# Kernel optimization log

Measured on AMD Instinct MI355X. Metric: run time of the kernel, lower is better.

The kernel has to match this reference:

```python
import math
import jax, jax.numpy as jnp
import numpy as np

B, L, D = 2, 2048, 1024
NH = 16
HS = D // NH
BLOCK_SIZE = 2048


def setup_inputs() -> dict:
    key = jax.random.key(0)
    ks = jax.random.split(key, 4)
    x = jax.random.normal(ks[0], (B, L, D), dtype=jnp.float32)
    Wqkv = jax.random.normal(ks[1], (D, 3 * D), dtype=jnp.float32) * 0.02
    bqkv = jnp.zeros((3 * D,), dtype=jnp.float32)
    Wproj = jax.random.normal(ks[2], (D, D), dtype=jnp.float32) * 0.02
    bproj = jnp.zeros((D,), dtype=jnp.float32)
    Er = jax.random.normal(ks[3], (BLOCK_SIZE, HS), dtype=jnp.float32)
    return {"x": x, "Wqkv": Wqkv, "bqkv": bqkv, "Wproj": Wproj, "bproj": bproj, "Er": Er}


def _skew(QEr):
    # QEr: [B, nh, L, L]  (Music Transformer skew trick)
    b, nh, nr, nc = QEr.shape
    padded = jnp.pad(QEr, ((0, 0), (0, 0), (0, 0), (1, 0)))  # [B, nh, nr, nc+1]
    reshaped = padded.reshape(b, nh, nc + 1, nr)
    return reshaped[:, :, 1:, :]  # [B, nh, nr, nc]


def reference(x, Wqkv, bqkv, Wproj, bproj, Er):
    b, l, d = x.shape
    qkv = x @ Wqkv + bqkv  # [B, L, 3D]
    q, k, v = jnp.split(qkv, 3, axis=2)
    q = q.reshape(b, l, NH, HS).transpose(0, 2, 1, 3)  # [B, nh, L, hs]
    k = k.reshape(b, l, NH, HS).transpose(0, 2, 1, 3)
    v = v.reshape(b, l, NH, HS).transpose(0, 2, 1, 3)

    start = BLOCK_SIZE - l
    Er_t = Er[start:, :].T  # [hs, L]
    QEr = jnp.einsum('bhld,dm->bhlm', q, Er_t)  # [B, nh, L, L]
    Srel = _skew(QEr)

    QK_t = jnp.einsum('bhld,bhmd->bhlm', q, k)
    scale = 1.0 / math.sqrt(HS)
    att = (QK_t + Srel) * scale
    causal = jnp.tril(jnp.ones((l, l), dtype=bool))
    att = jnp.where(causal[None, None, :, :], att, jnp.float32(-jnp.inf))
    att = jax.nn.softmax(att, axis=-1)
    y = jnp.einsum('bhlm,bhmd->bhld', att, v)
    y = y.transpose(0, 2, 1, 3).reshape(b, l, d)
    return y @ Wproj + bproj
```

## Files before the change

kernel.cpp:

```cpp
#include <hip/hip_runtime.h>
#include <stdint.h>

#define BB 2
#define LL 2048
#define DD 1024
#define NHH 16
#define HSS 64

typedef __bf16 bf16x8 __attribute__((ext_vector_type(8)));
typedef float f32x4 __attribute__((ext_vector_type(4)));

__device__ __forceinline__ bf16x8 load8(const float* p) {
  float4 f0 = *(const float4*)p;
  float4 f1 = *(const float4*)(p + 4);
  bf16x8 v;
  v[0] = (__bf16)f0.x; v[1] = (__bf16)f0.y; v[2] = (__bf16)f0.z; v[3] = (__bf16)f0.w;
  v[4] = (__bf16)f1.x; v[5] = (__bf16)f1.y; v[6] = (__bf16)f1.z; v[7] = (__bf16)f1.w;
  return v;
}
__device__ __forceinline__ bf16x8 load8(const __bf16* p) {
  return *(const bf16x8*)p;
}

template <typename T> struct raw8;
template <> struct raw8<float> {
  float4 lo, hi;
  __device__ __forceinline__ void load(const float* p) {
    lo = *(const float4*)p; hi = *(const float4*)(p + 4);
  }
  __device__ __forceinline__ bf16x8 cvt() const {
    bf16x8 v;
    v[0] = (__bf16)lo.x; v[1] = (__bf16)lo.y; v[2] = (__bf16)lo.z; v[3] = (__bf16)lo.w;
    v[4] = (__bf16)hi.x; v[5] = (__bf16)hi.y; v[6] = (__bf16)hi.z; v[7] = (__bf16)hi.w;
    return v;
  }
};
template <> struct raw8<__bf16> {
  bf16x8 v;
  __device__ __forceinline__ void load(const __bf16* p) { v = *(const bf16x8*)p; }
  __device__ __forceinline__ bf16x8 cvt() const { return v; }
};

__global__ void tconv_k(const float* __restrict__ src, __bf16* __restrict__ dst,
                        int R, int C) {
  __shared__ __bf16 tile[32][33];
  int c0 = blockIdx.x * 32, r0 = blockIdx.y * 32;
  int tx = threadIdx.x, ty = threadIdx.y;
#pragma unroll
  for (int i = ty; i < 32; i += 8)
    tile[i][tx] = (__bf16)src[(size_t)(r0 + i) * C + c0 + tx];
  __syncthreads();
#pragma unroll
  for (int i = ty; i < 32; i += 8)
    dst[(size_t)(c0 + i) * R + r0 + tx] = tile[tx][i];
}

template <typename AT>
__global__ __launch_bounds__(256, 3) void gemm128_k(
    const AT* __restrict__ A, const __bf16* __restrict__ Bt,
    const float* __restrict__ bias, int M, int N, int K, int mode,
    float* __restrict__ out, __bf16* __restrict__ Qo,
    __bf16* __restrict__ Ko, __bf16* __restrict__ Vto) {
  __shared__ __align__(16) __bf16 As[128 * 40];
  __shared__ __align__(16) __bf16 Bs[128 * 40];
  int t = threadIdx.x;
  int wave = t >> 6, lane = t & 63, qd = lane >> 4, lr = lane & 15;
  int m0 = blockIdx.y * 128, n0 = blockIdx.x * 128;
  int wm = (wave >> 1) * 64, wn = (wave & 1) * 64;
  f32x4 acc[4][4] = {};
  int sr = t >> 2, sc = (t & 3) * 8;
  const AT* Ap0 = A + (size_t)(m0 + sr) * K + sc;
  const AT* Ap1 = A + (size_t)(m0 + 64 + sr) * K + sc;
  const __bf16* Bp0 = Bt + (size_t)(n0 + sr) * K + sc;
  const __bf16* Bp1 = Bt + (size_t)(n0 + 64 + sr) * K + sc;

  raw8<AT> pa0, pa1;
  raw8<__bf16> pb0, pb1;
  pa0.load(Ap0); pa1.load(Ap1); pb0.load(Bp0); pb1.load(Bp1);

  for (int k0 = 0; k0 < K; k0 += 32) {
    __syncthreads();
    *(bf16x8*)&As[sr * 40 + sc] = pa0.cvt();
    *(bf16x8*)&As[(64 + sr) * 40 + sc] = pa1.cvt();
    *(bf16x8*)&Bs[sr * 40 + sc] = pb0.cvt();
    *(bf16x8*)&Bs[(64 + sr) * 40 + sc] = pb1.cvt();
    __syncthreads();
    if (k0 + 32 < K) {
      pa0.load(Ap0 + k0 + 32); pa1.load(Ap1 + k0 + 32);
      pb0.load(Bp0 + k0 + 32); pb1.load(Bp1 + k0 + 32);
    }
    bf16x8 af[4], bfr[4];
#pragma unroll
    for (int mt = 0; mt < 4; mt++)
      af[mt] = *(const bf16x8*)&As[(wm + mt * 16 + lr) * 40 + qd * 8];
#pragma unroll
    for (int nt = 0; nt < 4; nt++)
      bfr[nt] = *(const bf16x8*)&Bs[(wn + nt * 16 + lr) * 40 + qd * 8];
#pragma unroll
    for (int mt = 0; mt < 4; mt++)
#pragma unroll
      for (int nt = 0; nt < 4; nt++)
        acc[mt][nt] = __builtin_amdgcn_mfma_f32_16x16x32_bf16(af[mt], bfr[nt],
                                                              acc[mt][nt], 0, 0, 0);
  }
  float bvv[4];
#pragma unroll
  for (int nt = 0; nt < 4; nt++) bvv[nt] = bias[n0 + wn + nt * 16 + lr];
#pragma unroll
  for (int mt = 0; mt < 4; mt++) {
#pragma unroll
    for (int nt = 0; nt < 4; nt++) {
#pragma unroll
      for (int r = 0; r < 4; r++) {
        int row = m0 + wm + mt * 16 + qd * 4 + r;
        int col = n0 + wn + nt * 16 + lr;
        float v = acc[mt][nt][r] + bvv[nt];
        if (mode == 1) {
          out[(size_t)row * N + col] = v;
        } else {
          __bf16 bb = (__bf16)v;
          int b = row >> 11, l = row & 2047;
          if (col < DD) {
            int h = col >> 6, d = col & 63;
            Qo[(((size_t)(b * NHH + h)) * LL + l) * HSS + d] = bb;
          } else if (col < 2 * DD) {
            int c2 = col - DD;
            int h = c2 >> 6, d = c2 & 63;
            Ko[(((size_t)(b * NHH + h)) * LL + l) * HSS + d] = bb;
          } else {
            int c3 = col - 2 * DD;
            int h = c3 >> 6, d = c3 & 63;
            Vto[(((size_t)(b * NHH + h)) * HSS + d) * LL + l] = bb;
          }
        }
      }
    }
  }
}

__global__ __launch_bounds__(256, 2) void flash_k(
    const __bf16* __restrict__ Qg, const __bf16* __restrict__ Kg,
    const __bf16* __restrict__ Vtg, const float* __restrict__ Erg,
    __bf16* __restrict__ Yg) {
  __shared__ __align__(16) __bf16 Kld[64 * 72];
  __shared__ __align__(16) __bf16 Vld[80 * 72];
  __shared__ __align__(16) __bf16 Erld[128 * 72];
  __shared__ __align__(16) __bf16 Pball[4][16 * 72];

  int bh = blockIdx.y;
  const __bf16* Qh = Qg + (size_t)bh * LL * HSS;
  const __bf16* Kh = Kg + (size_t)bh * LL * HSS;
  const __bf16* Vth = Vtg + (size_t)bh * HSS * LL;
  int b = bh >> 4, h = bh & 15;
  int t = threadIdx.x, wave = t >> 6, lane = t & 63, qd = lane >> 4, lr = lane & 15;
  __bf16* Pb = &Pball[wave][0];
  int cbase = 48 - wave * 16;

  for (int idx = t; idx < 16 * 72; idx += 256) {
    int rr = idx / 72;
    Vld[(64 + rr) * 72 + (idx - rr * 72)] = (rr == 0) ? (__bf16)1.f : (__bf16)0.f;
  }

  int jj = t >> 2, hf = t & 3;
  int er = t >> 1, ec = (t & 1) * 32;

#pragma unroll 1
  for (int pass = 0; pass < 2; pass++) {
    int tile = (pass == 0) ? (int)blockIdx.x : (31 - (int)blockIdx.x);
    int i0 = tile * 64;

    bf16x8 aq[2];
    {
      const __bf16* qrow = Qh + (size_t)(i0 + wave * 16 + lr) * HSS + qd * 8;
      aq[0] = *(const bf16x8*)qrow;
      aq[1] = *(const bf16x8*)(qrow + 32);
    }
    f32x4 oacc[5] = {};

    bf16x8 kr0, kr1, vr0, vr1, ergs[4];
    auto prefetch = [&](int j0) {
      kr0 = *(const bf16x8*)&Kh[(size_t)(j0 + jj) * HSS + hf * 16];
      kr1 = *(const bf16x8*)&Kh[(size_t)(j0 + jj) * HSS + hf * 16 + 8];
      vr0 = *(const bf16x8*)&Vth[(size_t)jj * LL + j0 + hf * 16];
      vr1 = *(const bf16x8*)&Vth[(size_t)jj * LL + j0 + hf * 16 + 8];
      int e = LL - 64 - i0 + j0 + er;
      if (e < LL) {
#pragma unroll
        for (int kx = 0; kx < 4; kx++)
          ergs[kx] = load8(&Erg[(size_t)e * HSS + ec + kx * 8]);
      } else {
        bf16x8 z;
#pragma unroll
        for (int q = 0; q < 8; q++) z[q] = (__bf16)0.f;
#pragma unroll
        for (int kx = 0; kx < 4; kx++) ergs[kx] = z;
      }
    };
    prefetch(0);

    for (int j0 = 0; j0 <= i0; j0 += 64) {
      __syncthreads();
      *(bf16x8*)&Kld[jj * 72 + hf * 16] = kr0;
      *(bf16x8*)&Kld[jj * 72 + hf * 16 + 8] = kr1;
      *(bf16x8*)&Vld[jj * 72 + hf * 16] = vr0;
      *(bf16x8*)&Vld[jj * 72 + hf * 16 + 8] = vr1;
#pragma unroll
      for (int kx = 0; kx < 4; kx++)
        *(bf16x8*)&Erld[er * 72 + ec + kx * 8] = ergs[kx];
      __syncthreads();
      if (j0 + 64 <= i0) prefetch(j0 + 64);

      f32x4 sacc[4] = {};
#pragma unroll
      for (int ct = 0; ct < 4; ct++)
#pragma unroll
        for (int kc = 0; kc < 2; kc++) {
          bf16x8 bk = *(const bf16x8*)&Kld[(ct * 16 + lr) * 72 + kc * 32 + qd * 8];
          sacc[ct] = __builtin_amdgcn_mfma_f32_16x16x32_bf16(aq[kc], bk, sacc[ct], 0, 0, 0);
        }
      f32x4 racc[5] = {};
#pragma unroll
      for (int ct = 0; ct < 5; ct++)
#pragma unroll
        for (int kc = 0; kc < 2; kc++) {
          bf16x8 be = *(const bf16x8*)&Erld[(cbase + ct * 16 + lr) * 72 + kc * 32 + qd * 8];
          racc[ct] = __builtin_amdgcn_mfma_f32_16x16x32_bf16(aq[kc], be, racc[ct], 0, 0, 0);
        }

#pragma unroll
      for (int r = 0; r < 4; r++) {
        int tr = qd * 4 + r;
        int base = 15 - tr + lr;
        int src = qd * 16 + (base & 15);
        int hi = base >> 4;
        float sh[5];
#pragma unroll
        for (int ct = 0; ct < 5; ct++) sh[ct] = __shfl(racc[ct][r], src, 64);
        int gi = i0 + wave * 16 + tr;
#pragma unroll
        for (int ct2 = 0; ct2 < 4; ct2++) {
          float rel = hi ? sh[ct2 + 1] : sh[ct2];
          float s = (sacc[ct2][r] + rel) * 0.125f;
          int gj = j0 + ct2 * 16 + lr;
          float p = (gj <= gi) ? __expf(s) : 0.f;
          Pb[tr * 72 + ct2 * 16 + lr] = (__bf16)p;
        }
      }

      bf16x8 ap0 = *(const bf16x8*)&Pb[lr * 72 + qd * 8];
      bf16x8 ap1 = *(const bf16x8*)&Pb[lr * 72 + 32 + qd * 8];
#pragma unroll
      for (int dt = 0; dt < 5; dt++) {
        bf16x8 bv0 = *(const bf16x8*)&Vld[(dt * 16 + lr) * 72 + qd * 8];
        bf16x8 bv1 = *(const bf16x8*)&Vld[(dt * 16 + lr) * 72 + 32 + qd * 8];
        oacc[dt] = __builtin_amdgcn_mfma_f32_16x16x32_bf16(ap0, bv0, oacc[dt], 0, 0, 0);
        oacc[dt] = __builtin_amdgcn_mfma_f32_16x16x32_bf16(ap1, bv1, oacc[dt], 0, 0, 0);
      }
    }

#pragma unroll
    for (int r = 0; r < 4; r++) {
      float lv = __shfl(oacc[4][r], qd * 16, 64);
      float inv = 1.f / lv;
      int l = i0 + wave * 16 + qd * 4 + r;
#pragma unroll
      for (int dt = 0; dt < 4; dt++) {
        int d = dt * 16 + lr;
        Yg[((size_t)(b * LL) + l) * DD + h * HSS + d] = (__bf16)(oacc[dt][r] * inv);
      }
    }
  }
}

extern "C" void kernel_launch(void* const* d_in, const int* in_sizes, int n_in,
                              void* d_out, int out_size, void* d_ws, size_t ws_size,
                              hipStream_t stream) {
  const float* x = (const float*)d_in[0];
  const float* Wqkv = (const float*)d_in[1];
  const float* bqkv = (const float*)d_in[2];
  const float* Wproj = (const float*)d_in[3];
  const float* bproj = (const float*)d_in[4];
  const float* Er = (const float*)d_in[5];
  float* out = (float*)d_out;

  if (ws_size < 4u * 8388608u) return;

  uint8_t* w = (uint8_t*)d_ws;
  __bf16* Q = (__bf16*)w;  w += (size_t)BB * NHH * LL * HSS * 2;
  __bf16* Kt = (__bf16*)w; w += (size_t)BB * NHH * LL * HSS * 2;
  __bf16* Vt = (__bf16*)w; w += (size_t)BB * NHH * LL * HSS * 2;
  __bf16* Y = (__bf16*)w;  w += (size_t)BB * LL * DD * 2;

  __bf16* WqkvT = Y;
  __bf16* WprojT = Q;

  tconv_k<<<dim3(3072 / 32, 1024 / 32), dim3(32, 8), 0, stream>>>(Wqkv, WqkvT, 1024, 3072);
  gemm128_k<float><<<dim3(3072 / 128, 4096 / 128), 256, 0, stream>>>(
      x, WqkvT, bqkv, 4096, 3072, 1024, 0, nullptr, Q, Kt, Vt);
  flash_k<<<dim3(16, BB * NHH), 256, 0, stream>>>(Q, Kt, Vt, Er, Y);
  tconv_k<<<dim3(1024 / 32, 1024 / 32), dim3(32, 8), 0, stream>>>(Wproj, WprojT, 1024, 1024);
  gemm128_k<__bf16><<<dim3(1024 / 128, 4096 / 128), 256, 0, stream>>>(
      Y, WprojT, bproj, 4096, 1024, 1024, 1, out, nullptr, nullptr, nullptr);
}
```

Measured before the change: 261.5 us.

## Use async global-to-LDS loads in GEMMs and pre-convert inputs to bf16

Both projection GEMMs now stage A and B tiles through global_load_lds, copying straight into unpadded LDS instead of through registers. To make that possible, x is converted to bf16 in a combined prep kernel alongside the Wqkv transpose. V is written row-major to scratch in the output buffer and then transposed by a separate kernel instead of being scattered transposed from the GEMM epilogue. The output GEMM switches to 128x64 tiles for more blocks. The tradeoffs are lost register prefetch overlap (load then sync each k-step, single-buffered), possible LDS bank conflicts without padding, and extra kernel launches and passes over memory.

```diff
diff --git a/kernel.cpp b/kernel.cpp
--- a/kernel.cpp
+++ b/kernel.cpp
@@ -22,24 +22,33 @@
   return *(const bf16x8*)p;
 }
 
-template <typename T> struct raw8;
-template <> struct raw8<float> {
-  float4 lo, hi;
-  __device__ __forceinline__ void load(const float* p) {
-    lo = *(const float4*)p; hi = *(const float4*)(p + 4);
-  }
-  __device__ __forceinline__ bf16x8 cvt() const {
-    bf16x8 v;
-    v[0] = (__bf16)lo.x; v[1] = (__bf16)lo.y; v[2] = (__bf16)lo.z; v[3] = (__bf16)lo.w;
-    v[4] = (__bf16)hi.x; v[5] = (__bf16)hi.y; v[6] = (__bf16)hi.z; v[7] = (__bf16)hi.w;
-    return v;
-  }
-};
-template <> struct raw8<__bf16> {
-  bf16x8 v;
-  __device__ __forceinline__ void load(const __bf16* p) { v = *(const bf16x8*)p; }
-  __device__ __forceinline__ bf16x8 cvt() const { return v; }
-};
+__device__ __forceinline__ void async_ld16(__bf16* lds_uniform_base,
+                                           const __bf16* gptr_per_lane) {
+  __builtin_amdgcn_global_load_lds(
+      (const __attribute__((address_space(1))) void*)gptr_per_lane,
+      (__attribute__((address_space(3))) void*)lds_uniform_base, 16, 0, 0);
+}
+
+__global__ void prep_k(const float* __restrict__ Wqkv, const float* __restrict__ x,
+                       __bf16* __restrict__ WqkvT, __bf16* __restrict__ xb) {
+  __shared__ __bf16 tile[32][33];
+  int tx = threadIdx.x, ty = threadIdx.y;
+  if (blockIdx.z == 1) {
+    if (blockIdx.x >= 2048) return;
+    int tid = ty * 32 + tx;
+    size_t off = ((size_t)blockIdx.x * 256 + tid) * 8;
+    *(bf16x8*)&xb[off] = load8(&x[off]);
+    return;
+  }
+  int c0 = (blockIdx.x % 96) * 32, r0 = (blockIdx.x / 96) * 32;
+#pragma unroll
+  for (int i = ty; i < 32; i += 8)
+    tile[i][tx] = (__bf16)Wqkv[(size_t)(r0 + i) * 3072 + c0 + tx];
+  __syncthreads();
+#pragma unroll
+  for (int i = ty; i < 32; i += 8)
+    WqkvT[(size_t)(c0 + i) * 1024 + r0 + tx] = tile[tx][i];
+}
 
 __global__ void tconv_k(const float* __restrict__ src, __bf16* __restrict__ dst,
                         int R, int C) {
@@ -55,61 +64,78 @@
     dst[(size_t)(c0 + i) * R + r0 + tx] = tile[tx][i];
 }
 
-template <typename AT>
-__global__ __launch_bounds__(256, 3) void gemm128_k(
-    const AT* __restrict__ A, const __bf16* __restrict__ Bt,
+__global__ void vtrans_k(const __bf16* __restrict__ src, __bf16* __restrict__ dst) {
+  __shared__ __bf16 tile[32][33];
+  int bh = blockIdx.z;
+  int l0 = blockIdx.x * 32, d0 = blockIdx.y * 32;
+  const __bf16* s = src + (size_t)bh * LL * HSS;
+  __bf16* d = dst + (size_t)bh * HSS * LL;
+  int tx = threadIdx.x, ty = threadIdx.y;
+#pragma unroll
+  for (int i = ty; i < 32; i += 8)
+    tile[i][tx] = s[(size_t)(l0 + i) * HSS + d0 + tx];
+  __syncthreads();
+#pragma unroll
+  for (int i = ty; i < 32; i += 8)
+    d[(size_t)(d0 + i) * LL + l0 + tx] = tile[tx][i];
+}
+
+template <int NTILE>
+__global__ __launch_bounds__(256) void gemm_async_k(
+    const __bf16* __restrict__ A, const __bf16* __restrict__ Bt,
     const float* __restrict__ bias, int M, int N, int K, int mode,
     float* __restrict__ out, __bf16* __restrict__ Qo,
-    __bf16* __restrict__ Ko, __bf16* __restrict__ Vto) {
-  __shared__ __align__(16) __bf16 As[128 * 40];
-  __shared__ __align__(16) __bf16 Bs[128 * 40];
+    __bf16* __restrict__ Ko, __bf16* __restrict__ Vo) {
+  constexpr int NF = NTILE / 32;
+  constexpr int BG = NTILE / 64;
+  __shared__ __align__(16) __bf16 As[128 * 32];
+  __shared__ __align__(16) __bf16 Bs[NTILE * 32];
   int t = threadIdx.x;
   int wave = t >> 6, lane = t & 63, qd = lane >> 4, lr = lane & 15;
-  int m0 = blockIdx.y * 128, n0 = blockIdx.x * 128;
-  int wm = (wave >> 1) * 64, wn = (wave & 1) * 64;
-  f32x4 acc[4][4] = {};
-  int sr = t >> 2, sc = (t & 3) * 8;
-  const AT* Ap0 = A + (size_t)(m0 + sr) * K + sc;
-  const AT* Ap1 = A + (size_t)(m0 + 64 + sr) * K + sc;
-  const __bf16* Bp0 = Bt + (size_t)(n0 + sr) * K + sc;
-  const __bf16* Bp1 = Bt + (size_t)(n0 + 64 + sr) * K + sc;
-
-  raw8<AT> pa0, pa1;
-  raw8<__bf16> pb0, pb1;
-  pa0.load(Ap0); pa1.load(Ap1); pb0.load(Bp0); pb1.load(Bp1);
+  int m0 = blockIdx.y * 128, n0 = blockIdx.x * NTILE;
+  int wm = (wave >> 1) * 64, wn = (wave & 1) * (NTILE / 2);
+  f32x4 acc[4][NF] = {};
+  int srow = lane >> 2, sch = (lane & 3) * 8;
+
+  const __bf16* Ab[2];
+  const __bf16* Bb[BG];
+#pragma unroll
+  for (int c = 0; c < 2; c++)
+    Ab[c] = A + (size_t)(m0 + (wave * 2 + c) * 16 + srow) * K + sch;
+#pragma unroll
+  for (int c = 0; c < BG; c++)
+    Bb[c] = Bt + (size_t)(n0 + (wave * BG + c) * 16 + srow) * K + sch;
 
   for (int k0 = 0; k0 < K; k0 += 32) {
     __syncthreads();
-    *(bf16x8*)&As[sr * 40 + sc] = pa0.cvt();
-    *(bf16x8*)&As[(64 + sr) * 40 + sc] = pa1.cvt();
-    *(bf16x8*)&Bs[sr * 40 + sc] = pb0.cvt();
-    *(bf16x8*)&Bs[(64 + sr) * 40 + sc] = pb1.cvt();
+#pragma unroll
+    for (int c = 0; c < 2; c++)
+      async_ld16(&As[(wave * 2 + c) * 512], Ab[c] + k0);
+#pragma unroll
+    for (int c = 0; c < BG; c++)
+      async_ld16(&Bs[(wave * BG + c) * 512], Bb[c] + k0);
     __syncthreads();
-    if (k0 + 32 < K) {
-      pa0.load(Ap0 + k0 + 32); pa1.load(Ap1 + k0 + 32);
-      pb0.load(Bp0 + k0 + 32); pb1.load(Bp1 + k0 + 32);
-    }
-    bf16x8 af[4], bfr[4];
+    bf16x8 af[4], bfr[NF];
 #pragma unroll
     for (int mt = 0; mt < 4; mt++)
-      af[mt] = *(const bf16x8*)&As[(wm + mt * 16 + lr) * 40 + qd * 8];
-#pragma unroll
-    for (int nt = 0; nt < 4; nt++)
-      bfr[nt] = *(const bf16x8*)&Bs[(wn + nt * 16 + lr) * 40 + qd * 8];
+      af[mt] = *(const bf16x8*)&As[(wm + mt * 16 + lr) * 32 + qd * 8];
+#pragma unroll
+    for (int nt = 0; nt < NF; nt++)
+      bfr[nt] = *(const bf16x8*)&Bs[(wn + nt * 16 + lr) * 32 + qd * 8];
 #pragma unroll
     for (int mt = 0; mt < 4; mt++)
 #pragma unroll
-      for (int nt = 0; nt < 4; nt++)
+      for (int nt = 0; nt < NF; nt++)
         acc[mt][nt] = __builtin_amdgcn_mfma_f32_16x16x32_bf16(af[mt], bfr[nt],
                                                               acc[mt][nt], 0, 0, 0);
   }
-  float bvv[4];
-#pragma unroll
-  for (int nt = 0; nt < 4; nt++) bvv[nt] = bias[n0 + wn + nt * 16 + lr];
+  float bvv[NF];
+#pragma unroll
+  for (int nt = 0; nt < NF; nt++) bvv[nt] = bias[n0 + wn + nt * 16 + lr];
 #pragma unroll
   for (int mt = 0; mt < 4; mt++) {
 #pragma unroll
-    for (int nt = 0; nt < 4; nt++) {
+    for (int nt = 0; nt < NF; nt++) {
 #pragma unroll
       for (int r = 0; r < 4; r++) {
         int row = m0 + wm + mt * 16 + qd * 4 + r;
@@ -120,18 +146,9 @@
         } else {
           __bf16 bb = (__bf16)v;
           int b = row >> 11, l = row & 2047;
-          if (col < DD) {
-            int h = col >> 6, d = col & 63;
-            Qo[(((size_t)(b * NHH + h)) * LL + l) * HSS + d] = bb;
-          } else if (col < 2 * DD) {
-            int c2 = col - DD;
-            int h = c2 >> 6, d = c2 & 63;
-            Ko[(((size_t)(b * NHH + h)) * LL + l) * HSS + d] = bb;
-          } else {
-            int c3 = col - 2 * DD;
-            int h = c3 >> 6, d = c3 & 63;
-            Vto[(((size_t)(b * NHH + h)) * HSS + d) * LL + l] = bb;
-          }
+          int h = (col >> 6) & 15, d = col & 63;
+          __bf16* dst = (col < DD) ? Qo : (col < 2 * DD) ? Ko : Vo;
+          dst[(((size_t)(b * NHH + h)) * LL + l) * HSS + d] = bb;
         }
       }
     }
@@ -291,14 +308,17 @@
   __bf16* Vt = (__bf16*)w; w += (size_t)BB * NHH * LL * HSS * 2;
   __bf16* Y = (__bf16*)w;  w += (size_t)BB * LL * DD * 2;
 
-  __bf16* WqkvT = Y;
+  __bf16* xb = Y;
+  __bf16* WqkvT = (__bf16*)d_out;
+  __bf16* Vtmp = (__bf16*)((uint8_t*)d_out + (size_t)3072 * 1024 * 2);
   __bf16* WprojT = Q;
 
-  tconv_k<<<dim3(3072 / 32, 1024 / 32), dim3(32, 8), 0, stream>>>(Wqkv, WqkvT, 1024, 3072);
-  gemm128_k<float><<<dim3(3072 / 128, 4096 / 128), 256, 0, stream>>>(
-      x, WqkvT, bqkv, 4096, 3072, 1024, 0, nullptr, Q, Kt, Vt);
+  prep_k<<<dim3(3072, 1, 2), dim3(32, 8), 0, stream>>>(Wqkv, x, WqkvT, xb);
+  gemm_async_k<128><<<dim3(3072 / 128, 4096 / 128), 256, 0, stream>>>(
+      xb, WqkvT, bqkv, 4096, 3072, 1024, 0, nullptr, Q, Kt, Vtmp);
+  vtrans_k<<<dim3(LL / 32, HSS / 32, BB * NHH), dim3(32, 8), 0, stream>>>(Vtmp, Vt);
   flash_k<<<dim3(16, BB * NHH), 256, 0, stream>>>(Q, Kt, Vt, Er, Y);
   tconv_k<<<dim3(1024 / 32, 1024 / 32), dim3(32, 8), 0, stream>>>(Wproj, WprojT, 1024, 1024);
-  gemm128_k<__bf16><<<dim3(1024 / 128, 4096 / 128), 256, 0, stream>>>(
+  gemm_async_k<64><<<dim3(1024 / 64, 4096 / 128), 256, 0, stream>>>(
       Y, WprojT, bproj, 4096, 1024, 1024, 1, out, nullptr, nullptr, nullptr);
 }
```

Result: no change. 259.9 us (-0.6%).
